# Performance work log

Measured on AMD Instinct MI355X. Metric: run time of the kernel, lower is better.

The kernel has to match this reference:

```python
import jax, jax.numpy as jnp
import numpy as np
from jax import lax

EPS = 1e-5
K = 32  # k_neighbor

def conv1(x, w):
    # x: [B, Cin, L], w: [Cout, Cin] (1x1 conv, no bias)
    return jnp.einsum('bcl,oc->bol', x, w)

def bn(x, g, b):
    # BatchNorm1d in training mode: batch statistics over (batch, length)
    m = jnp.mean(x, axis=(0, 2), keepdims=True)
    v = jnp.var(x, axis=(0, 2), keepdims=True)
    return g[None, :, None] * (x - m) / jnp.sqrt(v + EPS) + b[None, :, None]

def res_block(x, w1, g1, b1, w2, g2, b2):
    h = jax.nn.gelu(bn(conv1(x, w1), g1, b1), approximate=False)
    h = bn(conv1(h, w2), g2, b2)
    return jax.nn.gelu(h + x, approximate=False)

def extraction(x, conv_w, bn_g, bn_b, fw, fg, fb):
    # conv_w: [n_blocks, 2, C, C]; bn_g/bn_b: [n_blocks, 2, C]
    for i in range(conv_w.shape[0]):
        x = res_block(x, conv_w[i, 0], bn_g[i, 0], bn_b[i, 0],
                      conv_w[i, 1], bn_g[i, 1], bn_b[i, 1])
    # TransformerBlock: ffn (conv+BN) with residual + GELU
    return jax.nn.gelu(x + bn(conv1(x, fw), fg, fb), approximate=False)

def setup_inputs() -> dict:
    key = jax.random.key(0)
    ks = jax.random.split(key, 16)
    B, N, S, C = 8, 4096, 1024, 128  # C = out_channel = 2*channel
    inp = {
        'xyz': jax.random.normal(ks[0], (B, N, 3), dtype=jnp.float32),
        'x': jax.random.normal(ks[1], (B, 64, N), dtype=jnp.float32),
        'fps_idx': jax.random.randint(ks[2], (B, S), 0, N, dtype=jnp.int64),
        'pre_conv_w': jax.random.normal(ks[3], (2, 2, C, C), dtype=jnp.float32) * 0.05,
        'pre_bn_g': jnp.ones((2, 2, C), jnp.float32),
        'pre_bn_b': jnp.zeros((2, 2, C), jnp.float32),
        'pre_ffn_w': jax.random.normal(ks[4], (C, C), dtype=jnp.float32) * 0.05,
        'pre_ffn_g': jnp.ones((C,), jnp.float32),
        'pre_ffn_b': jnp.zeros((C,), jnp.float32),
        'pos_conv_w': jax.random.normal(ks[5], (2, 2, C, C), dtype=jnp.float32) * 0.05,
        'pos_bn_g': jnp.ones((2, 2, C), jnp.float32),
        'pos_bn_b': jnp.zeros((2, 2, C), jnp.float32),
        'pos_ffn_w': jax.random.normal(ks[6], (C, C), dtype=jnp.float32) * 0.05,
        'pos_ffn_g': jnp.ones((C,), jnp.float32),
        'pos_ffn_b': jnp.zeros((C,), jnp.float32),
    }
    return inp

def reference(xyz, x, fps_idx,
              pre_conv_w, pre_bn_g, pre_bn_b, pre_ffn_w, pre_ffn_g, pre_ffn_b,
              pos_conv_w, pos_bn_g, pos_bn_b, pos_ffn_w, pos_ffn_g, pos_ffn_b):
    B, N, _ = xyz.shape
    S = fps_idx.shape[1]
    points = jnp.swapaxes(x, 1, 2)  # [B, N, d]
    d = points.shape[-1]

    # --- LocalGrouper ---
    new_xyz = jnp.take_along_axis(xyz, fps_idx[:, :, None], axis=1)      # [B, S, 3]
    new_pts = jnp.take_along_axis(points, fps_idx[:, :, None], axis=1)  # [B, S, d]

    # squared distances [B, S, N]
    sqr = (jnp.sum(new_xyz ** 2, -1)[:, :, None]
           + jnp.sum(xyz ** 2, -1)[:, None, :]
           - 2.0 * jnp.einsum('bsc,bnc->bsn', new_xyz, xyz))
    idx = lax.top_k(-sqr, K)[1]  # [B, S, K] smallest distances

    grouped = jnp.take_along_axis(points, idx.reshape(B, S * K)[:, :, None],
                                  axis=1).reshape(B, S, K, d)
    center = new_pts[:, :, None, :]  # [B, S, 1, d]
    feat = jnp.concatenate([grouped - center,
                            jnp.broadcast_to(center, grouped.shape)], axis=-1)  # [B,S,K,2d]

    C = 2 * d
    # --- PreExtraction: [B,S,K,C] -> [B*S, C, K] -> maxpool -> [B, C, S] ---
    y = jnp.swapaxes(feat, 2, 3).reshape(B * S, C, K)
    y = extraction(y, pre_conv_w, pre_bn_g, pre_bn_b, pre_ffn_w, pre_ffn_g, pre_ffn_b)
    y = jnp.max(y, axis=-1).reshape(B, S, C)
    y = jnp.swapaxes(y, 1, 2)  # [B, C, S]

    # --- PosExtraction ---
    y = extraction(y, pos_conv_w, pos_bn_g, pos_bn_b, pos_ffn_w, pos_ffn_g, pos_ffn_b)
    return (new_xyz, y)
```

## Files before the change

kernel.cpp:

```cpp
#include <hip/hip_runtime.h>
#include <math.h>

typedef unsigned short ushort_t;
typedef unsigned long long u64;
typedef unsigned int uint32;

#define B_ 8
#define N_ 4096
#define S_ 1024
#define K_ 32
#define C_ 128
#define NCOL1 (B_*S_*K_)
#define NCOL2 (B_*S_)
#define EPS_ 1e-5f

typedef ushort_t us8 __attribute__((ext_vector_type(8)));
typedef short s16x8 __attribute__((ext_vector_type(8)));
typedef float f32x4 __attribute__((ext_vector_type(4)));

__device__ __forceinline__ float bf2f(ushort_t u){ return __uint_as_float(((uint32)u)<<16); }
__device__ __forceinline__ ushort_t f2bf(float f){
    uint32 x = __float_as_uint(f);
    return (ushort_t)((x + 0x7FFFu + ((x>>16)&1u)) >> 16);
}
__device__ __forceinline__ float gelu_f(float v){
    float az = fabsf(v)*0.70710678118654752f;
    float t  = __builtin_amdgcn_rcpf(fmaf(0.3275911f, az, 1.0f));
    float p  = fmaf(fmaf(fmaf(fmaf(1.061405429f, t, -1.453152027f), t, 1.421413741f), t,
                   -0.284496736f), t, 0.254829592f)*t;
    float e  = __expf(-az*az);
    float er = fmaf(-p, e, 1.0f);
    float s  = (v < 0.0f) ? -er : er;
    return 0.5f*v*(1.0f+s);
}
__device__ __forceinline__ u64 shfl_xor_u64(u64 v, int m){
    int lo = __shfl_xor((int)(v & 0xFFFFFFFFull), m, 64);
    int hi = __shfl_xor((int)(v >> 32), m, 64);
    return (((u64)(uint32)hi) << 32) | (uint32)lo;
}

__global__ __launch_bounds__(256) void transpose_kernel(const float* __restrict__ x, float* __restrict__ xT){
    __shared__ float t[64][65];
    int b  = blockIdx.x >> 6;
    int n0 = (blockIdx.x & 63) * 64;
    int tx = threadIdx.x & 63, ty = threadIdx.x >> 6;
    #pragma unroll
    for (int i=0;i<16;i++){
        int c = i*4 + ty;
        t[c][tx] = x[((long)(b*64 + c))*N_ + n0 + tx];
    }
    __syncthreads();
    #pragma unroll
    for (int i=0;i<16;i++){
        int n = i*4 + ty;
        xT[((long)(b*N_ + n0 + n))*64 + tx] = t[tx][n];
    }
}

__global__ __launch_bounds__(256) void knn_kernel(const float* __restrict__ xyz, const int* __restrict__ fps,
                                                  int* __restrict__ idxg, float* __restrict__ newxyz){
    __shared__ uint32 hist[4096];
    __shared__ u64    cand[1024];
    __shared__ u64    out_keys[64];
    __shared__ uint32 csum[256];
    __shared__ uint32 wtot[4];
    __shared__ uint32 shv[8];
    __shared__ u64    wred[4];
    __shared__ u64    winner;

    int tid = threadIdx.x;
    int wv = tid >> 6, l = tid & 63;
    int bs = blockIdx.x;
    int b  = bs >> 10;
    int qi = fps[bs];
    const float* qb = xyz + ((long)b*N_ + qi)*3;
    float qx = qb[0], qy = qb[1], qz = qb[2];
    if (tid < 3) newxyz[(long)bs*3 + tid] = qb[tid];
    const float* xb = xyz + (long)b*N_*3;

    for (int i=tid;i<1024;i+=256) hist[i]=0;
    if (tid < 8) shv[tid]=0;
    __syncthreads();

    uint32 dbits[16];
    #pragma unroll
    for (int i=0;i<16;i++){
        int n = i*256 + tid;
        float dx = xb[n*3+0]-qx, dy = xb[n*3+1]-qy, dz = xb[n*3+2]-qz;
        float d = dx*dx + dy*dy + dz*dz;
        dbits[i] = __float_as_uint(d);
        atomicAdd(&hist[dbits[i]>>21], 1u);
    }
    __syncthreads();

    {
        uint32 h4[4]; uint32 csumv=0;
        #pragma unroll
        for (int i=0;i<4;i++){ h4[i]=hist[tid*4+i]; csumv+=h4[i]; }
        uint32 sc = csumv;
        #pragma unroll
        for (int off=1; off<64; off<<=1){ uint32 o=__shfl_up(sc,off,64); if (l>=off) sc+=o; }
        if (l==63) wtot[wv]=sc;
        csum[tid]=sc;
        __syncthreads();
        uint32 base=0;
        for (int w2=0; w2<wv; w2++) base += wtot[w2];
        uint32 cum = base + csum[tid] - csumv;
        #pragma unroll
        for (int i=0;i<4;i++){
            if (cum <= 31u && 31u < cum + h4[i]){ shv[0]=(uint32)(tid*4+i); shv[1]=cum; }
            cum += h4[i];
        }
    }
    __syncthreads();
    uint32 b1 = shv[0], cl1 = shv[1];

    for (int i=tid;i<4096;i+=256) hist[i]=0;
    __syncthreads();
    #pragma unroll
    for (int i=0;i<16;i++){
        uint32 u = dbits[i];
        if ((u>>21)==b1) atomicAdd(&hist[(u>>9)&0xFFFu], 1u);
    }
    __syncthreads();

    uint32 r2 = 31u - cl1;
    {
        uint32 h[16]; uint32 csumv=0;
        #pragma unroll
        for (int i=0;i<16;i++){ h[i]=hist[tid*16+i]; csumv += h[i]; }
        uint32 sc = csumv;
        #pragma unroll
        for (int off=1; off<64; off<<=1){ uint32 o=__shfl_up(sc,off,64); if (l>=off) sc+=o; }
        if (l==63) wtot[wv]=sc;
        csum[tid]=sc;
        __syncthreads();
        uint32 base=0;
        for (int w2=0; w2<wv; w2++) base += wtot[w2];
        uint32 cum = base + csum[tid] - csumv;
        #pragma unroll
        for (int i=0;i<16;i++){
            if (cum <= r2 && r2 < cum + h[i]){ shv[2]=(uint32)(tid*16+i); shv[3]=cum; }
            cum += h[i];
        }
    }
    __syncthreads();
    uint32 b2 = shv[2], cl2 = shv[3];
    uint32 nless = cl1 + cl2;

    #pragma unroll
    for (int i=0;i<16;i++){
        uint32 u = dbits[i];
        int n = i*256 + tid;
        uint32 bb1 = u >> 21;
        if (bb1 > b1) continue;
        u64 key = (((u64)u)<<32) | (uint32)n;
        if (bb1 < b1){
            uint32 p = atomicAdd(&shv[4],1u); out_keys[p] = key;
        } else {
            uint32 bb2 = (u>>9)&0xFFFu;
            if (bb2 < b2){ uint32 p = atomicAdd(&shv[4],1u); out_keys[p] = key; }
            else if (bb2 == b2){ uint32 p = atomicAdd(&shv[5],1u); if (p < 1024u) cand[p] = key; }
        }
    }
    __syncthreads();

    if (shv[5] > 1024u){
        uint32 alive = 0xFFFFu;
        for (int r=0;r<K_;r++){
            u64 lmin = ~0ull;
            #pragma unroll
            for (int i=0;i<16;i++){
                u64 k = (((u64)dbits[i])<<32) | (uint32)(i*256+tid);
                if (((alive>>i)&1u) && k < lmin) lmin = k;
            }
            #pragma unroll
            for (int off=32; off>=1; off>>=1){
                u64 o = shfl_xor_u64(lmin, off);
                if (o < lmin) lmin = o;
            }
            if (l == 0) wred[wv] = lmin;
            __syncthreads();
            if (tid == 0){
                u64 m = wred[0];
                if (wred[1]<m) m=wred[1];
                if (wred[2]<m) m=wred[2];
                if (wred[3]<m) m=wred[3];
                winner = m;
                idxg[(long)bs*K_ + r] = (int)(m & 0xFFFFFFFFull);
            }
            __syncthreads();
            u64 w = winner;
            #pragma unroll
            for (int i=0;i<16;i++){
                u64 k = (((u64)dbits[i])<<32) | (uint32)(i*256+tid);
                if (k == w) alive &= ~(1u<<i);
            }
        }
    } else if (wv == 0){
        uint32 cb   = shv[5];
        uint32 need = 32u - nless;
        for (uint32 r=0; r<need; r++){
            u64 lmin = ~0ull;
            for (uint32 s=l; s<cb; s+=64){ u64 kk = cand[s]; if (kk < lmin) lmin = kk; }
            #pragma unroll
            for (int off=32; off>=1; off>>=1){
                u64 o = shfl_xor_u64(lmin, off);
                if (o < lmin) lmin = o;
            }
            for (uint32 s=l; s<cb; s+=64){ if (cand[s]==lmin) cand[s] = ~0ull; }
            if (l==0) out_keys[nless + r] = lmin;
        }
        u64 key = (l < 32) ? out_keys[l] : ~0ull;
        #pragma unroll
        for (uint32 k=2; k<=64; k<<=1){
            bool dir = ((l & k)==0);
            #pragma unroll
            for (uint32 j=k>>1; j>=1; j>>=1){
                u64 o = shfl_xor_u64(key, j);
                bool lower = ((l & j)==0);
                u64 mn = (key < o) ? key : o;
                u64 mx = (key < o) ? o : key;
                key = (lower == dir) ? mn : mx;
            }
        }
        if (l < 32) idxg[(long)bs*K_ + l] = (int)(key & 0xFFFFFFFFull);
    }
}

__global__ __launch_bounds__(256) void build_kernel(const float* __restrict__ xT, const int* __restrict__ fps,
                                                    const int* __restrict__ idxg, ushort_t* __restrict__ A){
    long col = (long)blockIdx.x*256 + threadIdx.x;
    long bs  = col >> 5;
    int  b   = (int)(bs >> 10);
    int  n   = idxg[col];
    int  cn  = fps[bs];
    const float4* pr = (const float4*)(xT + ((long)b*N_ + n )*64);
    const float4* cr = (const float4*)(xT + ((long)b*N_ + cn)*64);
    ushort_t* op = A + col*C_;
    #pragma unroll
    for (int j=0;j<16;j++){
        float4 p = pr[j], c = cr[j];
        uint2 d, e;
        d.x = (((uint32)f2bf(p.y-c.y))<<16) | f2bf(p.x-c.x);
        d.y = (((uint32)f2bf(p.w-c.w))<<16) | f2bf(p.z-c.z);
        e.x = (((uint32)f2bf(c.y))<<16) | f2bf(c.x);
        e.y = (((uint32)f2bf(c.w))<<16) | f2bf(c.z);
        *(uint2*)(op + j*4)      = d;
        *(uint2*)(op + 64 + j*4) = e;
    }
}

__global__ __launch_bounds__(256) void wcvt_kernel(const float* __restrict__ pcw, const float* __restrict__ pfw,
                                                   const float* __restrict__ qcw, const float* __restrict__ qfw,
                                                   ushort_t* __restrict__ Wb){
    int i = blockIdx.x*256 + threadIdx.x;
    int mat = i >> 14;
    int r = i & 16383;
    float v;
    if (mat < 4)      v = pcw[i];
    else if (mat == 4) v = pfw[r];
    else if (mat < 9)  v = qcw[i - 5*16384];
    else               v = qfw[r];
    Wb[i] = f2bf(v);
}

template<int MODE, int PROLOG>
__global__ __launch_bounds__(256) void conv_mfma(const ushort_t* in1, const ushort_t* in2, ushort_t* aux,
                                                 ushort_t* out, const ushort_t* __restrict__ Wb,
                                                 const float* __restrict__ scsh_g, const float* __restrict__ pbprev,
                                                 const float* __restrict__ g, const float* __restrict__ bb,
                                                 float* __restrict__ pb, int nb, float inv_cnt){
    __shared__ float ss[256];
    __shared__ float sL[4][64], qL[4][64];
    int tid = threadIdx.x;
    int w = tid >> 6, l = tid & 63;
    int l15 = l & 15, l4 = l >> 4;

    if (MODE > 0){
        if (PROLOG){
            if (tid < 128){
                const float4* ps = (const float4*)(pbprev + tid*64);
                const float4* pq = (const float4*)(pbprev + (128+tid)*64);
                float s=0.f, q=0.f;
                #pragma unroll
                for (int i=0;i<16;i++){ float4 a=ps[i]; s += (a.x+a.y)+(a.z+a.w); }
                #pragma unroll
                for (int i=0;i<16;i++){ float4 a=pq[i]; q += (a.x+a.y)+(a.z+a.w); }
                float mean = s*inv_cnt, var = q*inv_cnt - mean*mean;
                float sc = g[tid]*rsqrtf(var+EPS_);
                ss[tid*2]   = sc;
                ss[tid*2+1] = bb[tid] - mean*sc;
            }
        } else {
            ss[tid] = scsh_g[tid];
        }
        __syncthreads();
    }

    int oc0 = (w & 1) << 6;
    long col0 = ((long)blockIdx.x << 7) + ((long)(w >> 1) << 6);

    f32x4 acc[4][4] = {};
    s16x8 keep[2][4];
    #pragma unroll
    for (int ks=0; ks<4; ks++){
        int kl = ks*32 + l4*8;
        s16x8 af[4];
        #pragma unroll
        for (int m=0;m<4;m++)
            af[m] = *(const s16x8*)(Wb + (oc0 + m*16 + l15)*C_ + kl);
        float sc[8], sh[8];
        if (MODE > 0){
            const float4* sp = (const float4*)(&ss[kl*2]);
            float4 s0 = sp[0], s1 = sp[1], s2 = sp[2], s3 = sp[3];
            sc[0]=s0.x; sh[0]=s0.y; sc[1]=s0.z; sh[1]=s0.w;
            sc[2]=s1.x; sh[2]=s1.y; sc[3]=s1.z; sh[3]=s1.w;
            sc[4]=s2.x; sh[4]=s2.y; sc[5]=s2.z; sh[5]=s2.w;
            sc[6]=s3.x; sh[6]=s3.y; sc[7]=s3.z; sh[7]=s3.w;
        }
        s16x8 bfr[4];
        #pragma unroll
        for (int n=0;n<4;n++){
            long cbase = (col0 + n*16 + l15)*C_ + kl;
            s16x8 v = *(const s16x8*)(in1 + cbase);
            if (MODE == 1){
                #pragma unroll
                for (int e=0;e<8;e++){
                    float f = gelu_f(fmaf(bf2f((ushort_t)v[e]), sc[e], sh[e]));
                    v[e] = (short)f2bf(f);
                }
            } else if (MODE == 2){
                s16x8 a = *(const s16x8*)(in2 + cbase);
                #pragma unroll
                for (int e=0;e<8;e++){
                    float f = gelu_f(fmaf(bf2f((ushort_t)v[e]), sc[e], sh[e]) + bf2f((ushort_t)a[e]));
                    v[e] = (short)f2bf(f);
                }
            }
            bfr[n] = v;
        }
        if (MODE == 2){
            if ((ks>>1) == (w&1)){
                #pragma unroll
                for (int n=0;n<4;n++) keep[ks&1][n] = bfr[n];
            }
        }
        #pragma unroll
        for (int m=0;m<4;m++)
            #pragma unroll
            for (int n=0;n<4;n++)
                acc[m][n] = __builtin_amdgcn_mfma_f32_16x16x32_bf16(af[m], bfr[n], acc[m][n], 0, 0, 0);
    }

    __syncthreads();

    if (MODE == 2){
        #pragma unroll
        for (int kk=0;kk<2;kk++){
            int ks = ((w&1)<<1) + kk;
            int kl = ks*32 + l4*8;
            #pragma unroll
            for (int n=0;n<4;n++)
                *(s16x8*)(aux + (col0 + n*16 + l15)*C_ + kl) = keep[kk][n];
        }
    }

    #pragma unroll
    for (int n=0;n<4;n++){
        long cadr = (col0 + n*16 + l15)*C_;
        #pragma unroll
        for (int m=0;m<4;m++){
            f32x4 a = acc[m][n];
            uint2 st;
            st.x = (((uint32)f2bf(a[1]))<<16) | f2bf(a[0]);
            st.y = (((uint32)f2bf(a[3]))<<16) | f2bf(a[2]);
            *(uint2*)(out + cadr + oc0 + m*16 + l4*4) = st;
        }
    }

    #pragma unroll
    for (int m=0;m<4;m++){
        #pragma unroll
        for (int r=0;r<4;r++){
            float a0=acc[m][0][r], a1=acc[m][1][r], a2=acc[m][2][r], a3=acc[m][3][r];
            float s = (a0+a1)+(a2+a3);
            float q = (a0*a0+a1*a1)+(a2*a2+a3*a3);
            #pragma unroll
            for (int off=1; off<16; off<<=1){
                s += __shfl_xor(s, off, 64);
                q += __shfl_xor(q, off, 64);
            }
            if (l15 == 0){
                sL[w][m*16 + l4*4 + r] = s;
                qL[w][m*16 + l4*4 + r] = q;
            }
        }
    }
    __syncthreads();
    if (tid < 128){
        int half = tid >> 6, rel = tid & 63;
        float s = sL[half][rel] + sL[half+2][rel];
        float q = qL[half][rel] + qL[half+2][rel];
        pb[(long)tid*nb + blockIdx.x]       = s;
        pb[(long)(128+tid)*nb + blockIdx.x] = q;
    }
}

__global__ __launch_bounds__(256) void reduce_fin_kernel(const float* __restrict__ pb, float* __restrict__ scsh,
                                                         const float* __restrict__ g, const float* __restrict__ bb,
                                                         float inv_cnt, int nb){
    int oc = blockIdx.x;
    float s=0.f, q=0.f;
    for (int b=threadIdx.x; b<nb; b+=256){
        s += pb[(long)oc*nb + b];
        q += pb[(long)(128+oc)*nb + b];
    }
    __shared__ float ls[256], lq[256];
    ls[threadIdx.x]=s; lq[threadIdx.x]=q;
    __syncthreads();
    #pragma unroll
    for (int st_=128; st_>0; st_>>=1){
        if (threadIdx.x < st_){ ls[threadIdx.x]+=ls[threadIdx.x+st_]; lq[threadIdx.x]+=lq[threadIdx.x+st_]; }
        __syncthreads();
    }
    if (threadIdx.x==0){
        float mean = ls[0]*inv_cnt;
        float var  = lq[0]*inv_cnt - mean*mean;
        float sc   = g[oc]*rsqrtf(var + EPS_);
        scsh[oc*2+0] = sc;
        scsh[oc*2+1] = bb[oc] - mean*sc;
    }
}

__global__ __launch_bounds__(256) void pool_kernel(const ushort_t* __restrict__ T, const ushort_t* __restrict__ X,
                                                   const float* __restrict__ scsh, ushort_t* __restrict__ A2){
    long p  = (long)blockIdx.x*256 + threadIdx.x;
    long bs = p >> 6;
    int  c0 = ((int)p & 63)*2;
    float sc0=scsh[c0*2], sh0=scsh[c0*2+1], sc1=scsh[c0*2+2], sh1=scsh[c0*2+3];
    const ushort_t* tb = T + (bs*K_)*(long)C_ + c0;
    const ushort_t* xv = X + (bs*K_)*(long)C_ + c0;
    float m0 = -1e30f, m1 = -1e30f;
    #pragma unroll 4
    for (int k=0;k<K_;k++){
        uint32 tv = *(const uint32*)(tb + (long)k*C_);
        uint32 av = *(const uint32*)(xv + (long)k*C_);
        float v0 = gelu_f(fmaf(bf2f((ushort_t)(tv & 0xFFFFu)), sc0, sh0) + bf2f((ushort_t)(av & 0xFFFFu)));
        float v1 = gelu_f(fmaf(bf2f((ushort_t)(tv >> 16)),     sc1, sh1) + bf2f((ushort_t)(av >> 16)));
        m0 = fmaxf(m0, v0);
        m1 = fmaxf(m1, v1);
    }
    uint32 o = (((uint32)f2bf(m1))<<16) | f2bf(m0);
    *(uint32*)(A2 + bs*C_ + c0) = o;
}

__global__ __launch_bounds__(256) void out_kernel(const ushort_t* __restrict__ T, const ushort_t* __restrict__ X,
                                                  const float* __restrict__ scsh, float* __restrict__ y){
    long o = (long)blockIdx.x*256 + threadIdx.x;
    int s = (int)(o & (S_-1));
    int c = (int)((o >> 10) & (C_-1));
    int b = (int)(o >> 17);
    long ad = ((long)(b*S_ + s))*C_ + c;
    float v = gelu_f(fmaf(bf2f(T[ad]), scsh[c*2], scsh[c*2+1]) + bf2f(X[ad]));
    y[o] = v;
}

extern "C" void kernel_launch(void* const* d_in, const int* in_sizes, int n_in,
                              void* d_out, int out_size, void* d_ws, size_t ws_size,
                              hipStream_t stream){
    const float* xyz        = (const float*)d_in[0];
    const float* x          = (const float*)d_in[1];
    const int*   fps        = (const int*)d_in[2];
    const float* pre_bn_g   = (const float*)d_in[4];
    const float* pre_bn_b   = (const float*)d_in[5];
    const float* pre_ffn_g  = (const float*)d_in[7];
    const float* pre_ffn_b  = (const float*)d_in[8];
    const float* pos_bn_g   = (const float*)d_in[10];
    const float* pos_bn_b   = (const float*)d_in[11];
    const float* pos_ffn_g  = (const float*)d_in[13];
    const float* pos_ffn_b  = (const float*)d_in[14];

    float* out_xyz = (float*)d_out;
    float* out_y   = (float*)d_out + (long)B_*S_*3;

    char* ws = (char*)d_ws;
    float*    scsh  = (float*)(ws + 0);
    float*    pb2a  = (float*)(ws + 10240);
    float*    pb2b  = (float*)(ws + 75776);
    ushort_t* Wb    = (ushort_t*)(ws + 141312);
    int*      idx   = (int*)(ws + 468992);
    float*    pb    = (float*)(ws + 468992);
    float*    xT    = (float*)(ws + 2566144);
    ushort_t* A2    = (ushort_t*)(ws + 2566144);
    ushort_t* C2    = (ushort_t*)(ws + 4663296);
    ushort_t* A1    = (ushort_t*)(ws + 10954752);
    ushort_t* Cb    = (ushort_t*)(ws + 78063616);
    (void)in_sizes; (void)n_in; (void)out_size; (void)ws_size;

    const float inv1 = 1.0f/(float)NCOL1, inv2 = 1.0f/(float)NCOL2;
    const ushort_t* Wp = Wb;
    const ushort_t* Wq = Wb + 5*C_*C_;

    wcvt_kernel<<<640,256,0,stream>>>((const float*)d_in[3], (const float*)d_in[6],
                                      (const float*)d_in[9], (const float*)d_in[12], Wb);
    transpose_kernel<<<B_*(N_/64),256,0,stream>>>(x, xT);
    knn_kernel<<<B_*S_,256,0,stream>>>(xyz, fps, idx, out_xyz);
    build_kernel<<<NCOL1/256,256,0,stream>>>(xT, fps, idx, A1);

    {
        int nb = NCOL1/128;
        const float* G[5]  = {pre_bn_g, pre_bn_g+C_, pre_bn_g+2*C_, pre_bn_g+3*C_, pre_ffn_g};
        const float* Bv[5] = {pre_bn_b, pre_bn_b+C_, pre_bn_b+2*C_, pre_bn_b+3*C_, pre_ffn_b};
        conv_mfma<0,0><<<nb,256,0,stream>>>(A1, nullptr, nullptr, Cb, Wp+0*C_*C_, nullptr, nullptr, nullptr, nullptr, pb, nb, inv1);
        reduce_fin_kernel<<<128,256,0,stream>>>(pb, scsh+0*256, G[0], Bv[0], inv1, nb);
        conv_mfma<1,0><<<nb,256,0,stream>>>(Cb, nullptr, nullptr, Cb, Wp+1*C_*C_, scsh+0*256, nullptr, nullptr, nullptr, pb, nb, inv1);
        reduce_fin_kernel<<<128,256,0,stream>>>(pb, scsh+1*256, G[1], Bv[1], inv1, nb);
        conv_mfma<2,0><<<nb,256,0,stream>>>(Cb, A1, A1, Cb, Wp+2*C_*C_, scsh+1*256, nullptr, nullptr, nullptr, pb, nb, inv1);
        reduce_fin_kernel<<<128,256,0,stream>>>(pb, scsh+2*256, G[2], Bv[2], inv1, nb);
        conv_mfma<1,0><<<nb,256,0,stream>>>(Cb, nullptr, nullptr, Cb, Wp+3*C_*C_, scsh+2*256, nullptr, nullptr, nullptr, pb, nb, inv1);
        reduce_fin_kernel<<<128,256,0,stream>>>(pb, scsh+3*256, G[3], Bv[3], inv1, nb);
        conv_mfma<2,0><<<nb,256,0,stream>>>(Cb, A1, A1, Cb, Wp+4*C_*C_, scsh+3*256, nullptr, nullptr, nullptr, pb, nb, inv1);
        reduce_fin_kernel<<<128,256,0,stream>>>(pb, scsh+4*256, G[4], Bv[4], inv1, nb);
        pool_kernel<<<(NCOL2*64)/256,256,0,stream>>>(Cb, A1, scsh+4*256, A2);
    }

    {
        int nb = NCOL2/128;
        const float* G[5]  = {pos_bn_g, pos_bn_g+C_, pos_bn_g+2*C_, pos_bn_g+3*C_, pos_ffn_g};
        const float* Bv[5] = {pos_bn_b, pos_bn_b+C_, pos_bn_b+2*C_, pos_bn_b+3*C_, pos_ffn_b};
        conv_mfma<0,1><<<nb,256,0,stream>>>(A2, nullptr, nullptr, C2, Wq+0*C_*C_, nullptr, nullptr, nullptr, nullptr, pb2a, nb, inv2);
        conv_mfma<1,1><<<nb,256,0,stream>>>(C2, nullptr, nullptr, C2, Wq+1*C_*C_, nullptr, pb2a, G[0], Bv[0], pb2b, nb, inv2);
        conv_mfma<2,1><<<nb,256,0,stream>>>(C2, A2, A2, C2, Wq+2*C_*C_, nullptr, pb2b, G[1], Bv[1], pb2a, nb, inv2);
        conv_mfma<1,1><<<nb,256,0,stream>>>(C2, nullptr, nullptr, C2, Wq+3*C_*C_, nullptr, pb2a, G[2], Bv[2], pb2b, nb, inv2);
        conv_mfma<2,1><<<nb,256,0,stream>>>(C2, A2, A2, C2, Wq+4*C_*C_, nullptr, pb2b, G[3], Bv[3], pb2a, nb, inv2);
        reduce_fin_kernel<<<128,256,0,stream>>>(pb2a, scsh+5*256, G[4], Bv[4], inv2, nb);
        out_kernel<<<(B_*C_*S_)/256,256,0,stream>>>(C2, A2, scsh+5*256, out_y);
    }
}
```

Before: 696.0 us.

## Give each wave all output channels over 32 columns to avoid duplicated prologue

Changes the per-wave tiling of the 1x1 conv MFMA kernel from a 64-channel by 64-column tile to all 128 output channels by 32 columns. Each input column is then loaded, BN-scaled and passed through GELU by one wave only, where before two waves both did this work. All input (and residual) fragments are loaded up front so their global memory latency overlaps. The cost is twice as many weight fragment loads per wave and higher register pressure, which could lower occupancy. The channel statistics reduction now sums across four waves.

Result: faster. 658.0 us (-5.5%).

```diff
diff --git a/kernel.cpp b/kernel.cpp
--- a/kernel.cpp
+++ b/kernel.cpp
@@ -272,7 +272,7 @@
                                                  const float* __restrict__ g, const float* __restrict__ bb,
                                                  float* __restrict__ pb, int nb, float inv_cnt){
     __shared__ float ss[256];
-    __shared__ float sL[4][64], qL[4][64];
+    __shared__ float sL[4][128], qL[4][128];
     int tid = threadIdx.x;
     int w = tid >> 6, l = tid & 63;
     int l15 = l & 15, l4 = l >> 4;
@@ -298,94 +298,88 @@
         __syncthreads();
     }
 
-    int oc0 = (w & 1) << 6;
-    long col0 = ((long)blockIdx.x << 7) + ((long)(w >> 1) << 6);
-
-    f32x4 acc[4][4] = {};
-    s16x8 keep[2][4];
+    long col0 = ((long)blockIdx.x << 7) + ((long)w << 5);
+
+    s16x8 bfr[8];
+    #pragma unroll
+    for (int t=0;t<8;t++){
+        int n = t>>2, ks = t&3;
+        bfr[t] = *(const s16x8*)(in1 + (col0 + n*16 + l15)*C_ + ks*32 + l4*8);
+    }
+    s16x8 a2[8];
+    if (MODE == 2){
+        #pragma unroll
+        for (int t=0;t<8;t++){
+            int n = t>>2, ks = t&3;
+            a2[t] = *(const s16x8*)(in2 + (col0 + n*16 + l15)*C_ + ks*32 + l4*8);
+        }
+    }
+
+    f32x4 acc[8][2] = {};
     #pragma unroll
     for (int ks=0; ks<4; ks++){
         int kl = ks*32 + l4*8;
-        s16x8 af[4];
-        #pragma unroll
-        for (int m=0;m<4;m++)
-            af[m] = *(const s16x8*)(Wb + (oc0 + m*16 + l15)*C_ + kl);
-        float sc[8], sh[8];
+        s16x8 af[8];
+        #pragma unroll
+        for (int m=0;m<8;m++)
+            af[m] = *(const s16x8*)(Wb + (m*16 + l15)*C_ + kl);
         if (MODE > 0){
+            float sc[8], sh[8];
             const float4* sp = (const float4*)(&ss[kl*2]);
             float4 s0 = sp[0], s1 = sp[1], s2 = sp[2], s3 = sp[3];
             sc[0]=s0.x; sh[0]=s0.y; sc[1]=s0.z; sh[1]=s0.w;
             sc[2]=s1.x; sh[2]=s1.y; sc[3]=s1.z; sh[3]=s1.w;
             sc[4]=s2.x; sh[4]=s2.y; sc[5]=s2.z; sh[5]=s2.w;
             sc[6]=s3.x; sh[6]=s3.y; sc[7]=s3.z; sh[7]=s3.w;
-        }
-        s16x8 bfr[4];
-        #pragma unroll
-        for (int n=0;n<4;n++){
-            long cbase = (col0 + n*16 + l15)*C_ + kl;
-            s16x8 v = *(const s16x8*)(in1 + cbase);
-            if (MODE == 1){
-                #pragma unroll
-                for (int e=0;e<8;e++){
-                    float f = gelu_f(fmaf(bf2f((ushort_t)v[e]), sc[e], sh[e]));
-                    v[e] = (short)f2bf(f);
+            #pragma unroll
+            for (int n=0;n<2;n++){
+                s16x8 v = bfr[n*4+ks];
+                if (MODE == 1){
+                    #pragma unroll
+                    for (int e=0;e<8;e++){
+                        float f = gelu_f(fmaf(bf2f((ushort_t)v[e]), sc[e], sh[e]));
+                        v[e] = (short)f2bf(f);
+                    }
+                } else {
+                    s16x8 a = a2[n*4+ks];
+                    #pragma unroll
+                    for (int e=0;e<8;e++){
+                        float f = gelu_f(fmaf(bf2f((ushort_t)v[e]), sc[e], sh[e]) + bf2f((ushort_t)a[e]));
+                        v[e] = (short)f2bf(f);
+                    }
                 }
-            } else if (MODE == 2){
-                s16x8 a = *(const s16x8*)(in2 + cbase);
-                #pragma unroll
-                for (int e=0;e<8;e++){
-                    float f = gelu_f(fmaf(bf2f((ushort_t)v[e]), sc[e], sh[e]) + bf2f((ushort_t)a[e]));
-                    v[e] = (short)f2bf(f);
-                }
-            }
-            bfr[n] = v;
-        }
-        if (MODE == 2){
-            if ((ks>>1) == (w&1)){
-                #pragma unroll
-                for (int n=0;n<4;n++) keep[ks&1][n] = bfr[n];
-            }
-        }
-        #pragma unroll
-        for (int m=0;m<4;m++)
-            #pragma unroll
-            for (int n=0;n<4;n++)
-                acc[m][n] = __builtin_amdgcn_mfma_f32_16x16x32_bf16(af[m], bfr[n], acc[m][n], 0, 0, 0);
-    }
-
-    __syncthreads();
-
-    if (MODE == 2){
-        #pragma unroll
-        for (int kk=0;kk<2;kk++){
-            int ks = ((w&1)<<1) + kk;
-            int kl = ks*32 + l4*8;
-            #pragma unroll
-            for (int n=0;n<4;n++)
-                *(s16x8*)(aux + (col0 + n*16 + l15)*C_ + kl) = keep[kk][n];
-        }
-    }
-
-    #pragma unroll
-    for (int n=0;n<4;n++){
+                bfr[n*4+ks] = v;
+                if (MODE == 2)
+                    *(s16x8*)(aux + (col0 + n*16 + l15)*C_ + kl) = v;
+            }
+        }
+        #pragma unroll
+        for (int m=0;m<8;m++)
+            #pragma unroll
+            for (int n=0;n<2;n++)
+                acc[m][n] = __builtin_amdgcn_mfma_f32_16x16x32_bf16(af[m], bfr[n*4+ks], acc[m][n], 0, 0, 0);
+    }
+
+    #pragma unroll
+    for (int n=0;n<2;n++){
         long cadr = (col0 + n*16 + l15)*C_;
         #pragma unroll
-        for (int m=0;m<4;m++){
+        for (int m=0;m<8;m++){
             f32x4 a = acc[m][n];
             uint2 st;
             st.x = (((uint32)f2bf(a[1]))<<16) | f2bf(a[0]);
             st.y = (((uint32)f2bf(a[3]))<<16) | f2bf(a[2]);
-            *(uint2*)(out + cadr + oc0 + m*16 + l4*4) = st;
-        }
-    }
-
-    #pragma unroll
-    for (int m=0;m<4;m++){
+            *(uint2*)(out + cadr + m*16 + l4*4) = st;
+        }
+    }
+
+    #pragma unroll
+    for (int m=0;m<8;m++){
         #pragma unroll
         for (int r=0;r<4;r++){
-            float a0=acc[m][0][r], a1=acc[m][1][r], a2=acc[m][2][r], a3=acc[m][3][r];
-            float s = (a0+a1)+(a2+a3);
-            float q = (a0*a0+a1*a1)+(a2*a2+a3*a3);
+            float a0=acc[m][0][r], a1=acc[m][1][r];
+            float s = a0+a1;
+            float q = a0*a0+a1*a1;
             #pragma unroll
             for (int off=1; off<16; off<<=1){
                 s += __shfl_xor(s, off, 64);
@@ -399,9 +393,8 @@
     }
     __syncthreads();
     if (tid < 128){
-        int half = tid >> 6, rel = tid & 63;
-        float s = sL[half][rel] + sL[half+2][rel];
-        float q = qL[half][rel] + qL[half+2][rel];
+        float s = sL[0][tid] + sL[1][tid] + sL[2][tid] + sL[3][tid];
+        float q = qL[0][tid] + qL[1][tid] + qL[2][tid] + qL[3][tid];
         pb[(long)tid*nb + blockIdx.x]       = s;
         pb[(long)(128+tid)*nb + blockIdx.x] = q;
     }
```
